# Performance work log

Hardware: AMD Instinct MI355X
Metric: run time of the kernel (lower is better)

Reference implementation:

```python
import jax, jax.numpy as jnp
import numpy as np

DIM = 1024

def setup_inputs() -> dict:
    key = jax.random.key(0)
    k1, k2, k3, k4, k5 = jax.random.split(key, 5)
    B, S, D = 32, 2048, DIM
    hidden_state = jax.random.normal(k1, (B, D), dtype=jnp.float32)
    encoder_outputs = jax.random.normal(k2, (B, S, D), dtype=jnp.float32)
    # linear1: (2D -> D) with bias; linear2: (D -> 1) no bias
    W1 = jax.random.normal(k3, (2 * D, D), dtype=jnp.float32) / np.sqrt(2 * D)
    b1 = jnp.zeros((D,), dtype=jnp.float32)
    w2 = jax.random.normal(k4, (D,), dtype=jnp.float32) / np.sqrt(D)
    return {"hidden_state": hidden_state, "encoder_outputs": encoder_outputs,
            "W1": W1, "b1": b1, "w2": w2}

def reference(hidden_state, encoder_outputs, W1, b1, w2):
    B, S, D = encoder_outputs.shape
    # concat(encoder_outputs, broadcast hidden) @ W1 == enc @ W1_enc + hid @ W1_hid
    W1_enc, W1_hid = W1[:D], W1[D:]                      # each [D, D]
    enc_proj = jnp.einsum('bsd,de->bse', encoder_outputs, W1_enc)
    hid_proj = jnp.einsum('bd,de->be', hidden_state, W1_hid)
    h = jnp.tanh(enc_proj + hid_proj[:, None, :] + b1)    # [B, S, D]
    e = jnp.einsum('bsd,d->bs', h, w2)                    # [B, S]
    alpha = jax.nn.softmax(e, axis=1)                     # [B, S]
    context = jnp.einsum('bs,bsd->bd', alpha, encoder_outputs)  # [B, D]
    return context
```

## Files before the change

### kernel.cpp

```cpp
#include <hip/hip_runtime.h>
#include <hip/hip_bf16.h>
#include <cstdint>

typedef __bf16 bf16;
typedef __bf16 bf16x4 __attribute__((ext_vector_type(4)));
typedef __bf16 bf16x8 __attribute__((ext_vector_type(8)));
typedef float  f32x4  __attribute__((ext_vector_type(4)));

#define N_ENCT   0u
#define N_W1BT   134217728u
#define N_C      136314880u
#define N_E      136445952u
#define N_ALPHA  136707072u
#define N_HIDP   136968192u
#define N_CTXP   138016768u
#define N_TOTAL  140113920ull

#define O_W1BT   0u
#define O_C      2097152u
#define O_E      2228224u
#define O_ALPHA  2490368u
#define O_HIDP   2752512u
#define O_CTXP   3801088u

__global__ __launch_bounds__(256) void k_convT(const float* __restrict__ in,
                                               bf16* __restrict__ encT) {
    __shared__ __align__(16) char lds[131072];
    const int t = threadIdx.x;
    const int mtg = blockIdx.x >> 2, q = blockIdx.x & 3;
    const float* src = in + (size_t)(mtg * 256 + q * 64) * 1024;
#pragma unroll 8
    for (int p = 0; p < 64; ++p) {
        f32x4 v = *(const f32x4*)(src + (size_t)p * 1024 + t * 4);
        bf16x4 o;
        o[0] = (bf16)v[0]; o[1] = (bf16)v[1]; o[2] = (bf16)v[2]; o[3] = (bf16)v[3];
        *(bf16x4*)(lds + p * 2048 + ((t * 8) ^ ((p & 7) << 4))) = o;
    }
    __syncthreads();
    char* dstb = (char*)encT + (size_t)mtg * 524288 + (size_t)q * 64 * 128;
#pragma unroll 2
    for (int kt = 0; kt < 16; ++kt) {
#pragma unroll
        for (int h = 0; h < 2; ++h) {
            int r = h * 32 + (t >> 3);
            f32x4 val = *(const f32x4*)(lds + r * 2048 + kt * 128 + (t & 7) * 16);
            *(f32x4*)(dstb + (size_t)kt * 32768 + r * 128 + (t & 7) * 16) = val;
        }
    }
}

__global__ void k_cvec_init(const float* __restrict__ b1, float* __restrict__ cvec) {
    int i = blockIdx.x * 256 + threadIdx.x;
    cvec[i] = b1[i & 1023];
}

__global__ void k_hid_atomic(const float* __restrict__ hid, const float* __restrict__ W1,
                             float* __restrict__ cvec) {
    int e = blockIdx.x * 256 + threadIdx.x;
    int dch = blockIdx.y;
    float acc[32];
#pragma unroll
    for (int b = 0; b < 32; ++b) acc[b] = 0.f;
    int d0 = dch * 32;
#pragma unroll 4
    for (int dd = 0; dd < 32; ++dd) {
        int d = d0 + dd;
        float w = W1[(size_t)(1024 + d) * 1024 + e];
#pragma unroll
        for (int b = 0; b < 32; ++b) acc[b] += hid[b * 1024 + d] * w;
    }
#pragma unroll
    for (int b = 0; b < 32; ++b) atomicAdd(&cvec[b * 1024 + e], acc[b]);
}

__global__ void k_hid_partial(const float* __restrict__ hid, const float* __restrict__ W1,
                              float* __restrict__ hidp) {
    int e = blockIdx.x * 256 + threadIdx.x;
    int dch = blockIdx.y;
    float acc[32];
#pragma unroll
    for (int b = 0; b < 32; ++b) acc[b] = 0.f;
    int d0 = dch * 128;
    for (int dd = 0; dd < 128; ++dd) {
        int d = d0 + dd;
        float w = W1[(size_t)(1024 + d) * 1024 + e];
#pragma unroll
        for (int b = 0; b < 32; ++b) acc[b] += hid[b * 1024 + d] * w;
    }
#pragma unroll
    for (int b = 0; b < 32; ++b) hidp[((size_t)dch * 32 + b) * 1024 + e] = acc[b];
}

__global__ void k_hid_reduce(const float* __restrict__ hidp, const float* __restrict__ b1,
                             float* __restrict__ cvec) {
    int i = blockIdx.x * 256 + threadIdx.x;
    int e = i & 1023;
    float s = b1[e];
#pragma unroll
    for (int dch = 0; dch < 8; ++dch) s += hidp[(size_t)dch * 32768 + i];
    cvec[i] = s;
}

__global__ void k_w1t(const float* __restrict__ W1, bf16* __restrict__ w1bt) {
    __shared__ float tile[32][33];
    int tx = threadIdx.x, ty = threadIdx.y;
    int bx = blockIdx.x, by = blockIdx.y;
#pragma unroll
    for (int i = 0; i < 4; ++i)
        tile[ty + i * 8][tx] = W1[(size_t)(by * 32 + ty + i * 8) * 1024 + bx * 32 + tx];
    __syncthreads();
#pragma unroll
    for (int i = 0; i < 4; ++i)
        w1bt[(size_t)(bx * 32 + ty + i * 8) * 1024 + by * 32 + tx] = (bf16)tile[tx][ty + i * 8];
}

__device__ inline float fast_tanh(float x) {
    float e2 = __expf(2.f * x);
    return 1.f - 2.f / (e2 + 1.f);
}

#define SBAR  __builtin_amdgcn_s_barrier()
#define LGKM0 asm volatile("s_waitcnt lgkmcnt(0)" ::: "memory")
#define VMC2  asm volatile("s_waitcnt vmcnt(2)" ::: "memory")
#define VMC4  asm volatile("s_waitcnt vmcnt(4)" ::: "memory")
#define PRIO1 __builtin_amdgcn_s_setprio(1)
#define PRIO0 __builtin_amdgcn_s_setprio(0)

template<int D, int MH>
__device__ __forceinline__ void rdA4(const char* p, bf16x8 (&bA)[4]) {
#pragma unroll
    for (int m = 0; m < 4; ++m)
        bA[m] = *(const bf16x8*)(p + D * 32768 + MH * 8192 + m * 2048);
}
template<int D>
__device__ __forceinline__ void rdB4(const char* p, bf16x8 (&bB)[4]) {
#pragma unroll
    for (int n = 0; n < 4; ++n)
        bB[n] = *(const bf16x8*)(p + D * 32768 + n * 2048);
}
template<int MH>
__device__ __forceinline__ void mfma16(bf16x8 (&bA)[4], bf16x8 (&bB)[4], f32x4 (&acc)[8][4]) {
#pragma unroll
    for (int m = 0; m < 4; ++m)
#pragma unroll
        for (int n = 0; n < 4; ++n)
            acc[MH * 4 + m][n] = __builtin_amdgcn_mfma_f32_16x16x32_bf16(
                bA[m], bB[n], acc[MH * 4 + m][n], 0, 0, 0);
}

__global__ __launch_bounds__(512, 1) void k_gemm8(
    const bf16* __restrict__ encT, const bf16* __restrict__ w1bt,
    const float* __restrict__ cvec, const float* __restrict__ w2,
    float* __restrict__ ebuf)
{
    __shared__ __align__(16) char smem[131072];
    const int t = threadIdx.x;
    const int lane = t & 63;
    const int w  = t >> 6;
    const int wr = w >> 2;
    const int wc = w & 3;
    const int l15 = lane & 15, g = (lane >> 4) & 3;

    unsigned bidx = blockIdx.x;
    unsigned swz0 = (bidx & 7u) * 128u + (bidx >> 3);
    const int nt  = swz0 & 3;
    const int mt0 = swz0 >> 2;
    const int n0  = nt * 256;

    const int r6  = t >> 3;
    const int gsl = (t & 7) ^ (r6 & 7);
    const char* tbAj = (const char*)encT + (size_t)mt0 * 524288;
    const char* srcB = (const char*)w1bt + (size_t)(n0 + r6) * 2048 + gsl * 16;

#define STAGE_A(TB, D, H, KT) do { \
    const char* _s = (TB) + (size_t)(KT) * 32768 + (H) * 16384 + t * 16; \
    __builtin_amdgcn_global_load_lds((const __attribute__((address_space(1))) unsigned int*)_s, \
        (__attribute__((address_space(3))) unsigned int*)(smem + (D) * 32768 + (H) * 16384 + w * 1024), 16, 0, 0); \
    __builtin_amdgcn_global_load_lds((const __attribute__((address_space(1))) unsigned int*)(_s + 8192), \
        (__attribute__((address_space(3))) unsigned int*)(smem + (D) * 32768 + (H) * 16384 + 8192 + w * 1024), 16, 0, 0); \
} while (0)
#define STAGE_B(D, H, KT) do { \
    const char* _s = srcB + (size_t)(H) * 262144 + (size_t)(KT) * 128; \
    __builtin_amdgcn_global_load_lds((const __attribute__((address_space(1))) unsigned int*)_s, \
        (__attribute__((address_space(3))) unsigned int*)(smem + 65536 + (D) * 32768 + (H) * 16384 + w * 1024), 16, 0, 0); \
    __builtin_amdgcn_global_load_lds((const __attribute__((address_space(1))) unsigned int*)(_s + 131072), \
        (__attribute__((address_space(3))) unsigned int*)(smem + 65536 + (D) * 32768 + (H) * 16384 + 8192 + w * 1024), 16, 0, 0); \
} while (0)

    const int rbA = wr * 128 + l15;
    const int rbB = wc * 64 + l15;
    const int sK0 = (g ^ (l15 & 7)) << 4;
    const int sK1 = sK0 ^ 64;
    const char* pA0 = smem + rbA * 128 + sK0;
    const char* pA1 = smem + rbA * 128 + sK1;
    const char* pB0 = smem + 65536 + rbB * 128 + sK0;
    const char* pB1 = smem + 65536 + rbB * 128 + sK1;

    f32x4 acc[8][4] = {};
    bf16x8 bA[4], bB[4];

    float wv[4];
    int gcol[4];
#pragma unroll
    for (int n = 0; n < 4; ++n) {
        gcol[n] = n0 + wc * 64 + n * 16 + l15;
        wv[n] = w2[gcol[n]];
    }

    STAGE_A(tbAj, 0, 0, 0); STAGE_A(tbAj, 0, 1, 0);
    STAGE_B(0, 0, 0); STAGE_B(0, 1, 0);
    STAGE_B(1, 0, 1); STAGE_B(1, 1, 1);
    VMC4; SBAR;

#pragma unroll 1
    for (int j = 0; j < 4; ++j) {
#pragma unroll 1
        for (int i = 0; i < 8; ++i) {
            const int st1 = 2 * i + 1;
            const int st2 = (2 * i + 2) & 15;
            const int st3 = (2 * i + 3) & 15;
            const char* tb2 = (i == 7) ? ((j < 3) ? tbAj + 4194304 : tbAj) : tbAj;

            rdA4<0, 0>(pA0, bA); rdB4<0>(pB0, bB);
            STAGE_A(tbAj, 1, 0, st1);
            SBAR; LGKM0; PRIO1; mfma16<0>(bA, bB, acc); PRIO0; SBAR;
            rdA4<0, 1>(pA0, bA);
            STAGE_A(tbAj, 1, 1, st1);
            SBAR; LGKM0; PRIO1; mfma16<1>(bA, bB, acc); PRIO0; SBAR;
            rdA4<0, 0>(pA1, bA); rdB4<0>(pB1, bB);
            SBAR; LGKM0; PRIO1; mfma16<0>(bA, bB, acc); PRIO0; SBAR;
            rdA4<0, 1>(pA1, bA);
            STAGE_B(0, 0, st2);
            SBAR; LGKM0; PRIO1; mfma16<1>(bA, bB, acc); PRIO0; VMC2; SBAR;
            rdA4<1, 0>(pA0, bA); rdB4<1>(pB0, bB);
            STAGE_B(0, 1, st2);
            SBAR; LGKM0; PRIO1; mfma16<0>(bA, bB, acc); PRIO0; SBAR;
            rdA4<1, 1>(pA0, bA);
            STAGE_A(tb2, 0, 0, st2);
            SBAR; LGKM0; PRIO1; mfma16<1>(bA, bB, acc); PRIO0; SBAR;
            rdA4<1, 0>(pA1, bA); rdB4<1>(pB1, bB);
            STAGE_A(tb2, 0, 1, st2);
            SBAR; LGKM0; PRIO1; mfma16<0>(bA, bB, acc); PRIO0; SBAR;
            rdA4<1, 1>(pA1, bA);
            STAGE_B(1, 0, st3); STAGE_B(1, 1, st3);
            SBAR; LGKM0; PRIO1; mfma16<1>(bA, bB, acc); PRIO0; VMC4; SBAR;
        }

        const int m0j = (mt0 + 8 * j) * 256;
        const int bj  = m0j >> 11;
        float cv[4];
#pragma unroll
        for (int n = 0; n < 4; ++n) cv[n] = cvec[bj * 1024 + gcol[n]];
#pragma unroll
        for (int m = 0; m < 8; ++m) {
#pragma unroll
            for (int r = 0; r < 4; ++r) {
                float s = 0.f;
#pragma unroll
                for (int n = 0; n < 4; ++n)
                    s += fast_tanh(acc[m][n][r] + cv[n]) * wv[n];
                s += __shfl_xor(s, 1); s += __shfl_xor(s, 2);
                s += __shfl_xor(s, 4); s += __shfl_xor(s, 8);
                if (l15 == 0)
                    atomicAdd(&ebuf[m0j + wr * 128 + m * 16 + g * 4 + r], s);
            }
        }
#pragma unroll
        for (int m = 0; m < 8; ++m)
#pragma unroll
            for (int n = 0; n < 4; ++n)
                acc[m][n] = f32x4{0.f, 0.f, 0.f, 0.f};

        tbAj += 4194304;
    }
#undef STAGE_A
#undef STAGE_B
}

__global__ __launch_bounds__(256, 3) void k_gemm_e(
    const float* __restrict__ enc, const bf16* __restrict__ w1bt,
    const float* __restrict__ cvec, const float* __restrict__ w2,
    float* __restrict__ ebuf)
{
    __shared__ __align__(16) unsigned char smem[24 * 1024];
    const int t = threadIdx.x;
    const int lane = t & 63;
    const int w = t >> 6;
    const int wr = w >> 1, wc = w & 1;
    const int l15 = lane & 15, g = lane >> 4;

    unsigned raw = blockIdx.x;
    unsigned swz = (raw & 7u) * 512u + (raw >> 3);
    const int nt = swz & 7, mt = swz >> 3;
    const int m0 = mt * 128, n0 = nt * 128;
    const int b = m0 >> 11;

    int rowA = (t >> 3);
    int slotA = (t & 7) ^ (rowA & 7);
    const char* gA0 = (const char*)enc + (size_t)(m0 + rowA) * 4096 + slotA * 16;
    int rowB = (t >> 2);
    int slotB = (t & 3) ^ ((t >> 3) & 3);
    const char* gB0 = (const char*)w1bt + (size_t)(n0 + rowB) * 2048 + slotB * 16;

    int rowA0 = wr * 64 + l15;
    unsigned offA0 = (unsigned)rowA0 * 128 + ((((2 * g)) ^ (l15 & 7)) << 4);
    int rowB0 = wc * 64 + l15;
    unsigned offB0 = 16384u + (unsigned)rowB0 * 64 + (((g ^ ((l15 >> 1) & 3))) << 4);

    f32x4 acc[4][4] = {};

    for (int kt = 0; kt < 32; ++kt) {
        const char* pa = gA0 + kt * 128;
        const char* pb = gB0 + kt * 64;
#pragma unroll
        for (int c = 0; c < 4; ++c)
            __builtin_amdgcn_global_load_lds(
                (const __attribute__((address_space(1))) unsigned int*)(pa + (size_t)c * 131072),
                (__attribute__((address_space(3))) unsigned int*)(smem + c * 4096 + w * 1024), 16, 0, 0);
#pragma unroll
        for (int c = 0; c < 2; ++c)
            __builtin_amdgcn_global_load_lds(
                (const __attribute__((address_space(1))) unsigned int*)(pb + (size_t)c * 131072),
                (__attribute__((address_space(3))) unsigned int*)(smem + 16384 + c * 4096 + w * 1024), 16, 0, 0);
        __syncthreads();

        bf16x8 af[4], bfr[4];
#pragma unroll
        for (int m = 0; m < 4; ++m) {
            unsigned o0 = offA0 + m * 2048;
            f32x4 lo = *(const f32x4*)(smem + o0);
            f32x4 hi = *(const f32x4*)(smem + (o0 ^ 16u));
            bf16x8 a;
            a[0] = (bf16)lo[0]; a[1] = (bf16)lo[1]; a[2] = (bf16)lo[2]; a[3] = (bf16)lo[3];
            a[4] = (bf16)hi[0]; a[5] = (bf16)hi[1]; a[6] = (bf16)hi[2]; a[7] = (bf16)hi[3];
            af[m] = a;
        }
#pragma unroll
        for (int n = 0; n < 4; ++n)
            bfr[n] = *(const bf16x8*)(smem + (offB0 + n * 1024));
#pragma unroll
        for (int m = 0; m < 4; ++m)
#pragma unroll
            for (int n = 0; n < 4; ++n)
                acc[m][n] = __builtin_amdgcn_mfma_f32_16x16x32_bf16(af[m], bfr[n], acc[m][n], 0, 0, 0);
        __syncthreads();
    }

    float cv[4], wv[4];
#pragma unroll
    for (int n = 0; n < 4; ++n) {
        int gcol = n0 + wc * 64 + n * 16 + l15;
        cv[n] = cvec[b * 1024 + gcol];
        wv[n] = w2[gcol];
    }
#pragma unroll
    for (int m = 0; m < 4; ++m) {
#pragma unroll
        for (int r = 0; r < 4; ++r) {
            float s = 0.f;
#pragma unroll
            for (int n = 0; n < 4; ++n)
                s += fast_tanh(acc[m][n][r] + cv[n]) * wv[n];
            s += __shfl_xor(s, 1); s += __shfl_xor(s, 2);
            s += __shfl_xor(s, 4); s += __shfl_xor(s, 8);
            if (l15 == 0)
                atomicAdd(&ebuf[m0 + wr * 64 + m * 16 + g * 4 + r], s);
        }
    }
}

__global__ void k_softmax(const float* __restrict__ ebuf, float* __restrict__ alpha) {
    int bb = blockIdx.x, t = threadIdx.x;
    __shared__ float red[4], red2[4];
    float v[8];
    float mx = -1e30f;
#pragma unroll
    for (int i = 0; i < 8; ++i) { v[i] = ebuf[bb * 2048 + i * 256 + t]; mx = fmaxf(mx, v[i]); }
    for (int o = 32; o > 0; o >>= 1) mx = fmaxf(mx, __shfl_xor(mx, o));
    if ((t & 63) == 0) red[t >> 6] = mx;
    __syncthreads();
    mx = fmaxf(fmaxf(red[0], red[1]), fmaxf(red[2], red[3]));
    float sum = 0.f;
#pragma unroll
    for (int i = 0; i < 8; ++i) { v[i] = __expf(v[i] - mx); sum += v[i]; }
    for (int o = 32; o > 0; o >>= 1) sum += __shfl_xor(sum, o);
    if ((t & 63) == 0) red2[t >> 6] = sum;
    __syncthreads();
    sum = red2[0] + red2[1] + red2[2] + red2[3];
    float inv = 1.f / sum;
#pragma unroll
    for (int i = 0; i < 8; ++i) alpha[bb * 2048 + i * 256 + t] = v[i] * inv;
}

__global__ void k_ctx_t(const bf16* __restrict__ encT, const float* __restrict__ alpha,
                        float* __restrict__ ctxp) {
    int bid = blockIdx.x;
    int bb = bid >> 4, sc = bid & 15;
    int t = threadIdx.x;
    __shared__ float al[128];
    __shared__ float red[1024];
    if (t < 128) al[t] = alpha[bb * 2048 + sc * 128 + t];
    __syncthreads();
    int j = t & 127, kt = j >> 3, sL = j & 7, sp = t >> 7;
    int mtg = bb * 8 + (sc >> 1);
    int rbase = (sc & 1) * 128;
    const char* base = (const char*)encT + (size_t)mtg * 524288 + (size_t)kt * 32768;
    float acc[8] = {};
    for (int ri = 0; ri < 64; ++ri) {
        int rr = rbase + ri * 2 + sp;
        bf16x8 v = *(const bf16x8*)(base + rr * 128 + ((sL ^ (rr & 7)) << 4));
        float a = al[ri * 2 + sp];
#pragma unroll
        for (int k = 0; k < 8; ++k) acc[k] += a * (float)v[k];
    }
    if (sp == 1) {
#pragma unroll
        for (int k = 0; k < 8; ++k) red[j * 8 + k] = acc[k];
    }
    __syncthreads();
    if (sp == 0) {
        float* o = ctxp + (size_t)bid * 1024 + j * 8;
#pragma unroll
        for (int k = 0; k < 8; ++k) o[k] = acc[k] + red[j * 8 + k];
    }
}

__global__ void k_ctx_partial(const float* __restrict__ enc, const float* __restrict__ alpha,
                              float* __restrict__ ctxp) {
    int bid = blockIdx.x;
    int bb = bid >> 4, sc = bid & 15;
    int t = threadIdx.x;
    __shared__ float al[128];
    if (t < 128) al[t] = alpha[bb * 2048 + sc * 128 + t];
    __syncthreads();
    f32x4 acc = {0.f, 0.f, 0.f, 0.f};
    const f32x4* base = (const f32x4*)(enc + ((size_t)bb * 2048 + sc * 128) * 1024) + t;
    for (int s = 0; s < 128; ++s) {
        f32x4 vv = base[(size_t)s * 256];
        acc += vv * al[s];
    }
    *((f32x4*)(ctxp + (size_t)bid * 1024) + t) = acc;
}

__global__ void k_ctx_reduce(const float* __restrict__ ctxp, float* __restrict__ out) {
    int i = blockIdx.x * 256 + threadIdx.x;
    int bb = i >> 10, d = i & 1023;
    float s = 0.f;
#pragma unroll
    for (int sc = 0; sc < 16; ++sc) s += ctxp[((size_t)(bb * 16 + sc)) * 1024 + d];
    out[i] = s;
}

extern "C" void kernel_launch(void* const* d_in, const int* in_sizes, int n_in,
                              void* d_out, int out_size, void* d_ws, size_t ws_size,
                              hipStream_t stream) {
    const float* hid = (const float*)d_in[0];
    const float* enc = (const float*)d_in[1];
    const float* W1  = (const float*)d_in[2];
    const float* b1  = (const float*)d_in[3];
    const float* w2  = (const float*)d_in[4];
    float* out = (float*)d_out;
    char* ws = (char*)d_ws;

    if (ws_size >= N_TOTAL) {
        bf16*  encT  = (bf16*)(ws + N_ENCT);
        bf16*  w1bt  = (bf16*)(ws + N_W1BT);
        float* cvec  = (float*)(ws + N_C);
        float* ebuf  = (float*)(ws + N_E);
        float* alpha = (float*)(ws + N_ALPHA);
        float* ctxp  = (float*)(ws + N_CTXP);

        hipMemsetAsync(ebuf, 0, 65536 * sizeof(float), stream);
        k_convT<<<1024, 256, 0, stream>>>(enc, encT);
        k_w1t<<<dim3(32, 32), dim3(32, 8), 0, stream>>>(W1, w1bt);
        k_cvec_init<<<128, 256, 0, stream>>>(b1, cvec);
        k_hid_atomic<<<dim3(4, 32), 256, 0, stream>>>(hid, W1, cvec);
        k_gemm8<<<256, 512, 0, stream>>>(encT, w1bt, cvec, w2, ebuf);
        k_softmax<<<32, 256, 0, stream>>>(ebuf, alpha);
        k_ctx_t<<<512, 256, 0, stream>>>(encT, alpha, ctxp);
        k_ctx_reduce<<<128, 256, 0, stream>>>(ctxp, out);
    } else {
        bf16*  w1bt  = (bf16*)(ws + O_W1BT);
        float* cvec  = (float*)(ws + O_C);
        float* ebuf  = (float*)(ws + O_E);
        float* alpha = (float*)(ws + O_ALPHA);
        float* hidp  = (float*)(ws + O_HIDP);
        float* ctxp  = (float*)(ws + O_CTXP);

        hipMemsetAsync(ebuf, 0, 65536 * sizeof(float), stream);
        k_hid_partial<<<dim3(4, 8), 256, 0, stream>>>(hid, W1, hidp);
        k_w1t<<<dim3(32, 32), dim3(32, 8), 0, stream>>>(W1, w1bt);
        k_hid_reduce<<<128, 256, 0, stream>>>(hidp, b1, cvec);
        k_gemm_e<<<4096, 256, 0, stream>>>(enc, w1bt, cvec, w2, ebuf);
        k_softmax<<<32, 256, 0, stream>>>(ebuf, alpha);
        k_ctx_partial<<<512, 256, 0, stream>>>(enc, alpha, ctxp);
        k_ctx_reduce<<<128, 256, 0, stream>>>(ctxp, out);
    }
}
```

Measured before the change: 281.2 us.

## Double-buffer LDS fragment registers to overlap ds_reads with MFMA in GEMM loop

Introduces two sets of A/B fragment registers so the LDS reads for the next MFMA block are issued before the current MFMA block runs, instead of reading then waiting. Adds sched_barrier fences and reorders the barrier, waitcnt and global-to-LDS staging points around the prefetched reads, and splits the last B stage across two phases with an adjusted vmcnt. The intent is to hide LDS read latency behind matrix core work. In exchange it raises register pressure and carries a risk of LDS read-after-write hazards if the barrier placement is wrong.

Measured after the change: 289.0 us. +2.7%, slower.

```diff
diff --git a/kernel.cpp b/kernel.cpp
--- a/kernel.cpp
+++ b/kernel.cpp
@@ -119,33 +119,34 @@
     return 1.f - 2.f / (e2 + 1.f);
 }
 
-#define SBAR  __builtin_amdgcn_s_barrier()
-#define LGKM0 asm volatile("s_waitcnt lgkmcnt(0)" ::: "memory")
-#define VMC2  asm volatile("s_waitcnt vmcnt(2)" ::: "memory")
-#define VMC4  asm volatile("s_waitcnt vmcnt(4)" ::: "memory")
-#define PRIO1 __builtin_amdgcn_s_setprio(1)
-#define PRIO0 __builtin_amdgcn_s_setprio(0)
+#define SBAR   __builtin_amdgcn_s_barrier()
+#define SCHED0 __builtin_amdgcn_sched_barrier(0)
+#define LGKM0  asm volatile("s_waitcnt lgkmcnt(0)" ::: "memory")
+#define VMC2   asm volatile("s_waitcnt vmcnt(2)" ::: "memory")
+#define VMC4   asm volatile("s_waitcnt vmcnt(4)" ::: "memory")
+#define PRIO1  __builtin_amdgcn_s_setprio(1)
+#define PRIO0  __builtin_amdgcn_s_setprio(0)
 
 template<int D, int MH>
-__device__ __forceinline__ void rdA4(const char* p, bf16x8 (&bA)[4]) {
+__device__ __forceinline__ void rdA4(const char* p, bf16x8 (&o)[4]) {
 #pragma unroll
     for (int m = 0; m < 4; ++m)
-        bA[m] = *(const bf16x8*)(p + D * 32768 + MH * 8192 + m * 2048);
+        o[m] = *(const bf16x8*)(p + D * 32768 + MH * 8192 + m * 2048);
 }
 template<int D>
-__device__ __forceinline__ void rdB4(const char* p, bf16x8 (&bB)[4]) {
+__device__ __forceinline__ void rdB4(const char* p, bf16x8 (&o)[4]) {
 #pragma unroll
     for (int n = 0; n < 4; ++n)
-        bB[n] = *(const bf16x8*)(p + D * 32768 + n * 2048);
+        o[n] = *(const bf16x8*)(p + D * 32768 + n * 2048);
 }
 template<int MH>
-__device__ __forceinline__ void mfma16(bf16x8 (&bA)[4], bf16x8 (&bB)[4], f32x4 (&acc)[8][4]) {
+__device__ __forceinline__ void mfma16(bf16x8 (&fa)[4], bf16x8 (&fb)[4], f32x4 (&acc)[8][4]) {
 #pragma unroll
     for (int m = 0; m < 4; ++m)
 #pragma unroll
         for (int n = 0; n < 4; ++n)
             acc[MH * 4 + m][n] = __builtin_amdgcn_mfma_f32_16x16x32_bf16(
-                bA[m], bB[n], acc[MH * 4 + m][n], 0, 0, 0);
+                fa[m], fb[n], acc[MH * 4 + m][n], 0, 0, 0);
 }
 
 __global__ __launch_bounds__(512, 1) void k_gemm8(
@@ -197,7 +198,7 @@
     const char* pB1 = smem + 65536 + rbB * 128 + sK1;
 
     f32x4 acc[8][4] = {};
-    bf16x8 bA[4], bB[4];
+    bf16x8 fa0[4], fa1[4], fb0[4], fb1[4];
 
     float wv[4];
     int gcol[4];
@@ -211,6 +212,7 @@
     STAGE_B(0, 0, 0); STAGE_B(0, 1, 0);
     STAGE_B(1, 0, 1); STAGE_B(1, 1, 1);
     VMC4; SBAR;
+    rdA4<0, 0>(pA0, fa0); rdB4<0>(pB0, fb0);
 
 #pragma unroll 1
     for (int j = 0; j < 4; ++j) {
@@ -221,29 +223,56 @@
             const int st3 = (2 * i + 3) & 15;
             const char* tb2 = (i == 7) ? ((j < 3) ? tbAj + 4194304 : tbAj) : tbAj;
 
-            rdA4<0, 0>(pA0, bA); rdB4<0>(pB0, bB);
+            LGKM0; SCHED0;
+            rdA4<0, 1>(pA0, fa1);
+            SBAR;
             STAGE_A(tbAj, 1, 0, st1);
-            SBAR; LGKM0; PRIO1; mfma16<0>(bA, bB, acc); PRIO0; SBAR;
-            rdA4<0, 1>(pA0, bA);
+            PRIO1; mfma16<0>(fa0, fb0, acc); PRIO0;
+            SBAR;
+            LGKM0; SCHED0;
+            rdA4<0, 0>(pA1, fa0); rdB4<0>(pB1, fb1);
+            SBAR;
             STAGE_A(tbAj, 1, 1, st1);
-            SBAR; LGKM0; PRIO1; mfma16<1>(bA, bB, acc); PRIO0; SBAR;
-            rdA4<0, 0>(pA1, bA); rdB4<0>(pB1, bB);
-            SBAR; LGKM0; PRIO1; mfma16<0>(bA, bB, acc); PRIO0; SBAR;
-            rdA4<0, 1>(pA1, bA);
+            PRIO1; mfma16<1>(fa1, fb0, acc); PRIO0;
+            SBAR;
+            LGKM0; SCHED0;
+            rdA4<0, 1>(pA1, fa1);
+            SBAR;
             STAGE_B(0, 0, st2);
-            SBAR; LGKM0; PRIO1; mfma16<1>(bA, bB, acc); PRIO0; VMC2; SBAR;
-            rdA4<1, 0>(pA0, bA); rdB4<1>(pB0, bB);
+            PRIO1; mfma16<0>(fa0, fb1, acc); PRIO0;
+            VMC2;
+            SBAR;
+            LGKM0; SCHED0;
+            rdA4<1, 0>(pA0, fa0); rdB4<1>(pB0, fb0);
+            SBAR;
             STAGE_B(0, 1, st2);
-            SBAR; LGKM0; PRIO1; mfma16<0>(bA, bB, acc); PRIO0; SBAR;
-            rdA4<1, 1>(pA0, bA);
+            PRIO1; mfma16<1>(fa1, fb1, acc); PRIO0;
+            SBAR;
+            LGKM0; SCHED0;
+            rdA4<1, 1>(pA0, fa1);
+            SBAR;
             STAGE_A(tb2, 0, 0, st2);
-            SBAR; LGKM0; PRIO1; mfma16<1>(bA, bB, acc); PRIO0; SBAR;
-            rdA4<1, 0>(pA1, bA); rdB4<1>(pB1, bB);
+            PRIO1; mfma16<0>(fa0, fb0, acc); PRIO0;
+            SBAR;
+            LGKM0; SCHED0;
+            rdA4<1, 0>(pA1, fa0); rdB4<1>(pB1, fb1);
+            SBAR;
             STAGE_A(tb2, 0, 1, st2);
-            SBAR; LGKM0; PRIO1; mfma16<0>(bA, bB, acc); PRIO0; SBAR;
-            rdA4<1, 1>(pA1, bA);
-            STAGE_B(1, 0, st3); STAGE_B(1, 1, st3);
-            SBAR; LGKM0; PRIO1; mfma16<1>(bA, bB, acc); PRIO0; VMC4; SBAR;
+            PRIO1; mfma16<1>(fa1, fb0, acc); PRIO0;
+            SBAR;
+            LGKM0; SCHED0;
+            rdA4<1, 1>(pA1, fa1);
+            SBAR;
+            STAGE_B(1, 0, st3);
+            PRIO1; mfma16<0>(fa0, fb1, acc); PRIO0;
+            VMC2;
+            SBAR;
+            LGKM0; SCHED0;
+            rdA4<0, 0>(pA0, fa0); rdB4<0>(pB0, fb0);
+            SBAR;
+            STAGE_B(1, 1, st3);
+            PRIO1; mfma16<1>(fa1, fb1, acc); PRIO0;
+            SBAR;
         }
 
         const int m0j = (mt0 + 8 * j) * 256;
```
